# Performance work log

Hardware: AMD Instinct MI355X
Metric: run time of the kernel (lower is better)

## Reference

```python
import jax, jax.numpy as jnp
import numpy as np

F, H, D, A, B = 500, 2000, 64, 64, 4096


def setup_inputs() -> dict:
    key = jax.random.key(0)
    ks = jax.random.split(key, 6)
    values = jax.random.normal(ks[0], (B, F), dtype=jnp.float32)
    feat_emb = jax.random.normal(ks[1], (F, D), dtype=jnp.float32) * 0.02
    hid_emb = jax.random.normal(ks[2], (H, D), dtype=jnp.float32) * 0.02
    Ww = jax.random.normal(ks[3], (2 * D, A), dtype=jnp.float32) * (1.0 / np.sqrt(2 * D))
    bw = jnp.zeros((A,), dtype=jnp.float32)
    Wu = jax.random.normal(ks[4], (A, 1), dtype=jnp.float32) * (1.0 / np.sqrt(A))
    mask = jax.random.bernoulli(ks[5], 0.1, (F, F + H, 1))
    return {"values": values, "feat_emb": feat_emb, "hid_emb": hid_emb,
            "Ww": Ww, "bw": bw, "Wu": Wu, "mask": mask}


def reference(values, feat_emb, hid_emb, Ww, bw, Wu, mask):
    d = feat_emb.shape[1]
    # full embedding matrix: concat(feature, hidden) -> [F+H, d]
    full = jnp.concatenate([feat_emb, hid_emb], axis=0)
    # Dense(tanh) on concat([feat_emb tiled, full tiled], axis=2) == split-weight form:
    # avoids materializing the [F, F+H, 2d] concat tensor (same math).
    W1, W2 = Ww[:d], Ww[d:]
    pre_f = feat_emb @ W1          # [F, A]
    pre_w = full @ W2              # [F+H, A]
    h = jnp.tanh(pre_f[:, None, :] + pre_w[None, :, :] + bw)  # [F, F+H, A]
    score = h @ Wu                 # [F, F+H, 1]
    # masked exp-normalize (not a stable softmax: original uses raw exp)
    score = jnp.where(mask, jnp.exp(score), 0.0)
    ssum = jnp.sum(score, axis=1, keepdims=True)        # [F, 1, 1]
    ssum = jnp.where(ssum == 0, 1.0, ssum)
    attn = score / ssum                                  # [F, F+H, 1]
    context = jnp.sum(attn * full[None, :, :], axis=1)   # [F, d]
    return values @ context                              # [B, d]
```

## Files before the change

kernel.cpp:

```cpp
#include <hip/hip_runtime.h>
#include <cstdint>
#include <cstddef>

#define F_N 500
#define H_N 2000
#define JN  2500
#define D_N 64
#define A_N 64
#define B_N 4096

__global__ __launch_bounds__(256) void k_pre(
    const float* __restrict__ feat, const float* __restrict__ hid,
    const float* __restrict__ Ww,   const float* __restrict__ bw,
    float* __restrict__ pre_f, float* __restrict__ pre_w)
{
    const int lane = threadIdx.x & 63;
    const int wave = threadIdx.x >> 6;
    const int row  = blockIdx.x * 4 + wave;
    if (row >= F_N + JN) return;

    const float* emb;
    const float* W;
    float*       outp;
    float        acc = 0.0f;

    if (row < F_N) {
        emb  = feat + (size_t)row * D_N;
        W    = Ww;
        outp = pre_f + (size_t)row * A_N;
        acc  = bw[lane];
    } else {
        const int j = row - F_N;
        emb  = (j < F_N) ? (feat + (size_t)j * D_N)
                         : (hid + (size_t)(j - F_N) * D_N);
        W    = Ww + D_N * A_N;
        outp = pre_w + (size_t)j * A_N;
    }

    const float e = emb[lane];
    #pragma unroll 16
    for (int d = 0; d < D_N; ++d) {
        const float w = W[d * A_N + lane];
        const float b = __shfl(e, d, 64);
        acc = fmaf(b, w, acc);
    }
    outp[lane] = acc;
}

__global__ __launch_bounds__(256) void k_attn(
    const float* __restrict__ feat, const float* __restrict__ hid,
    const float* __restrict__ pre_f, const float* __restrict__ pre_w,
    const float* __restrict__ Wu,   const void* __restrict__ mask,
    float* __restrict__ ctx)
{
    const int lane = threadIdx.x & 63;
    const int wave = threadIdx.x >> 6;
    const int i    = blockIdx.x;

    const uint32_t* mw = (const uint32_t*)mask;
    const uint32_t probe = mw[lane] | mw[64 + lane] | mw[128 + lane] | mw[192 + lane];
    const bool byteMode = (__ballot(probe > 1u) != 0ull);

    const float pf = pre_f[(size_t)i * A_N + lane];
    const float wu = Wu[lane];

    const uint8_t*  mb = (const uint8_t*)mask + (size_t)i * JN;
    const uint32_t* mi = (const uint32_t*)mask + (size_t)i * JN;

    float cacc = 0.0f;
    float sacc = 0.0f;

    for (int c = wave; c < 40; c += 4) {
        const int j0 = c * 64;
        const int j  = j0 + lane;
        uint32_t m = 0;
        if (j < JN) m = byteMode ? (uint32_t)mb[j] : mi[j];
        unsigned long long act = __ballot(m != 0);

        while (act) {
            const int b0 = __builtin_ctzll(act); act &= act - 1;
            const bool has1 = (act != 0ull);
            const int b1 = has1 ? __builtin_ctzll(act) : b0;
            if (has1) act &= act - 1;
            const int jj0 = j0 + b0;
            const int jj1 = j0 + b1;

            const float x0 = pf + pre_w[(size_t)jj0 * A_N + lane];
            const float x1 = pf + pre_w[(size_t)jj1 * A_N + lane];
            const float t0 = 1.0f - 2.0f / (__expf(2.0f * x0) + 1.0f);
            const float t1 = 1.0f - 2.0f / (__expf(2.0f * x1) + 1.0f);
            float p0 = t0 * wu;
            float p1 = t1 * wu;
            #pragma unroll
            for (int off = 1; off < 64; off <<= 1) {
                p0 += __shfl_xor(p0, off, 64);
                p1 += __shfl_xor(p1, off, 64);
            }
            const float e0 = __expf(p0);
            const float e1 = has1 ? __expf(p1) : 0.0f;
            sacc += e0 + e1;

            const float f0 = (jj0 < F_N) ? feat[(size_t)jj0 * D_N + lane]
                                         : hid[(size_t)(jj0 - F_N) * D_N + lane];
            const float f1 = (jj1 < F_N) ? feat[(size_t)jj1 * D_N + lane]
                                         : hid[(size_t)(jj1 - F_N) * D_N + lane];
            cacc = fmaf(e0, f0, cacc);
            cacc = fmaf(e1, f1, cacc);
        }
    }

    __shared__ float s_ctx[4][64];
    __shared__ float s_sum[4];
    s_ctx[wave][lane] = cacc;
    if (lane == 0) s_sum[wave] = sacc;
    __syncthreads();
    if (wave == 0) {
        const float c4 = s_ctx[0][lane] + s_ctx[1][lane] + s_ctx[2][lane] + s_ctx[3][lane];
        float s = s_sum[0] + s_sum[1] + s_sum[2] + s_sum[3];
        if (s == 0.0f) s = 1.0f;
        ctx[(size_t)i * D_N + lane] = c4 / s;
    }
}

__global__ __launch_bounds__(256) void k_out(
    const float* __restrict__ values, const float* __restrict__ ctx,
    float* __restrict__ out)
{
    const int lane = threadIdx.x & 63;
    const int wave = threadIdx.x >> 6;
    const int row0 = blockIdx.x * 8 + wave * 2;

    __shared__ float lds[100 * 64];
    float acc0 = 0.0f, acc1 = 0.0f;

    for (int chunk = 0; chunk < 5; ++chunk) {
        const int k0 = chunk * 100;
        __syncthreads();
        for (int t = threadIdx.x; t < 100 * 64; t += 256)
            lds[t] = ctx[(size_t)k0 * 64 + t];
        __syncthreads();

        const float* v0p = values + (size_t)row0 * 500 + k0;
        const float* v1p = v0p + 500;
        #pragma unroll 5
        for (int kc = 0; kc < 100; kc += 4) {
            const float4 a = *(const float4*)(v0p + kc);
            const float4 b = *(const float4*)(v1p + kc);
            const float l0 = lds[(kc + 0) * 64 + lane];
            const float l1 = lds[(kc + 1) * 64 + lane];
            const float l2 = lds[(kc + 2) * 64 + lane];
            const float l3 = lds[(kc + 3) * 64 + lane];
            acc0 = fmaf(a.x, l0, acc0); acc0 = fmaf(a.y, l1, acc0);
            acc0 = fmaf(a.z, l2, acc0); acc0 = fmaf(a.w, l3, acc0);
            acc1 = fmaf(b.x, l0, acc1); acc1 = fmaf(b.y, l1, acc1);
            acc1 = fmaf(b.z, l2, acc1); acc1 = fmaf(b.w, l3, acc1);
        }
    }
    out[(size_t)row0 * 64 + lane]       = acc0;
    out[(size_t)(row0 + 1) * 64 + lane] = acc1;
}

extern "C" void kernel_launch(void* const* d_in, const int* in_sizes, int n_in,
                              void* d_out, int out_size, void* d_ws, size_t ws_size,
                              hipStream_t stream)
{
    const float* values = (const float*)d_in[0];
    const float* feat   = (const float*)d_in[1];
    const float* hid    = (const float*)d_in[2];
    const float* Ww     = (const float*)d_in[3];
    const float* bw     = (const float*)d_in[4];
    const float* Wu     = (const float*)d_in[5];
    const void*  mask   = d_in[6];
    float* out = (float*)d_out;

    float* wsf   = (float*)d_ws;
    float* pre_f = wsf;
    float* pre_w = wsf + 32000;
    float* ctx   = wsf + 192000;

    k_pre <<<750, 256, 0, stream>>>(feat, hid, Ww, bw, pre_f, pre_w);
    k_attn<<<500, 256, 0, stream>>>(feat, hid, pre_f, pre_w, Wu, mask, ctx);
    k_out <<<512, 256, 0, stream>>>(values, ctx, out);
}
```

Measured before the change: 132.5 us.

## Transpose pre_w and compute attention scores one-per-thread over compacted mask list

k_pre now has each wave compute four rows and writes pre_w transposed through an LDS tile. k_attn first compacts the active mask indices into a shared list using ballot and atomics. Each thread then computes a full 64-wide tanh score for one active index, reading pre_w with coalesced transposed loads, instead of doing a wave-wide shuffle reduction per index. This removes the per-index butterfly reductions and the serial per-wave loop, at the cost of extra LDS use, more synchronization, and a nondeterministic list order that changes the float summation order.

```diff
diff --git a/kernel.cpp b/kernel.cpp
--- a/kernel.cpp
+++ b/kernel.cpp
@@ -9,116 +9,152 @@
 #define A_N 64
 #define B_N 4096
 
-__global__ __launch_bounds__(256) void k_pre(
+__global__ __launch_bounds__(1024) void k_pre(
     const float* __restrict__ feat, const float* __restrict__ hid,
     const float* __restrict__ Ww,   const float* __restrict__ bw,
-    float* __restrict__ pre_f, float* __restrict__ pre_w)
+    float* __restrict__ pre_f, float* __restrict__ pre_wT)
 {
     const int lane = threadIdx.x & 63;
     const int wave = threadIdx.x >> 6;
-    const int row  = blockIdx.x * 4 + wave;
-    if (row >= F_N + JN) return;
-
-    const float* emb;
-    const float* W;
-    float*       outp;
-    float        acc = 0.0f;
-
-    if (row < F_N) {
-        emb  = feat + (size_t)row * D_N;
-        W    = Ww;
-        outp = pre_f + (size_t)row * A_N;
-        acc  = bw[lane];
-    } else {
-        const int j = row - F_N;
-        emb  = (j < F_N) ? (feat + (size_t)j * D_N)
-                         : (hid + (size_t)(j - F_N) * D_N);
-        W    = Ww + D_N * A_N;
-        outp = pre_w + (size_t)j * A_N;
-    }
-
-    const float e = emb[lane];
-    #pragma unroll 16
+
+    __shared__ float tile[64 * 65];
+
+    const bool isPreF = (blockIdx.x < 8);
+    const int  rbase  = isPreF ? blockIdx.x * 64 : (blockIdx.x - 8) * 64;
+    const int  r0     = rbase + wave * 4;
+    const int  rowLim = isPreF ? F_N : JN;
+
+    const float* W = isPreF ? Ww : (Ww + D_N * A_N);
+
+    float acc0, acc1, acc2, acc3;
+    if (isPreF) { const float b = bw[lane]; acc0 = acc1 = acc2 = acc3 = b; }
+    else        { acc0 = acc1 = acc2 = acc3 = 0.0f; }
+
+    float e0 = 0.f, e1 = 0.f, e2 = 0.f, e3 = 0.f;
+    {
+        const int r[4] = { r0, r0 + 1, r0 + 2, r0 + 3 };
+        float* ep[4] = { &e0, &e1, &e2, &e3 };
+        #pragma unroll
+        for (int q = 0; q < 4; ++q) {
+            const int rr = r[q];
+            if (rr < rowLim) {
+                const float* emb;
+                if (isPreF)          emb = feat + (size_t)rr * D_N;
+                else if (rr < F_N)   emb = feat + (size_t)rr * D_N;
+                else                 emb = hid + (size_t)(rr - F_N) * D_N;
+                *ep[q] = emb[lane];
+            }
+        }
+    }
+
+    #pragma unroll
     for (int d = 0; d < D_N; ++d) {
         const float w = W[d * A_N + lane];
-        const float b = __shfl(e, d, 64);
-        acc = fmaf(b, w, acc);
-    }
-    outp[lane] = acc;
+        acc0 = fmaf(__shfl(e0, d, 64), w, acc0);
+        acc1 = fmaf(__shfl(e1, d, 64), w, acc1);
+        acc2 = fmaf(__shfl(e2, d, 64), w, acc2);
+        acc3 = fmaf(__shfl(e3, d, 64), w, acc3);
+    }
+
+    if (isPreF) {
+        if (r0 + 0 < F_N) pre_f[(size_t)(r0 + 0) * A_N + lane] = acc0;
+        if (r0 + 1 < F_N) pre_f[(size_t)(r0 + 1) * A_N + lane] = acc1;
+        if (r0 + 2 < F_N) pre_f[(size_t)(r0 + 2) * A_N + lane] = acc2;
+        if (r0 + 3 < F_N) pre_f[(size_t)(r0 + 3) * A_N + lane] = acc3;
+    } else {
+        const int l0 = wave * 4;
+        tile[(l0 + 0) * 65 + lane] = acc0;
+        tile[(l0 + 1) * 65 + lane] = acc1;
+        tile[(l0 + 2) * 65 + lane] = acc2;
+        tile[(l0 + 3) * 65 + lane] = acc3;
+        __syncthreads();
+        #pragma unroll
+        for (int k = 0; k < 4; ++k) {
+            const int idx = threadIdx.x + k * 1024;
+            const int a   = idx >> 6;
+            const int jj  = idx & 63;
+            const int j   = rbase + jj;
+            if (j < JN)
+                pre_wT[(size_t)a * JN + j] = tile[jj * 65 + a];
+        }
+    }
 }
 
 __global__ __launch_bounds__(256) void k_attn(
     const float* __restrict__ feat, const float* __restrict__ hid,
-    const float* __restrict__ pre_f, const float* __restrict__ pre_w,
+    const float* __restrict__ pre_f, const float* __restrict__ pre_wT,
     const float* __restrict__ Wu,   const void* __restrict__ mask,
     float* __restrict__ ctx)
 {
-    const int lane = threadIdx.x & 63;
-    const int wave = threadIdx.x >> 6;
+    const int tid  = threadIdx.x;
+    const int lane = tid & 63;
+    const int wave = tid >> 6;
     const int i    = blockIdx.x;
+
+    __shared__ int   list[JN];
+    __shared__ float earr[JN];
+    __shared__ float s_ctx[4][64];
+    __shared__ int   nact;
+
+    if (tid == 0) nact = 0;
+    __syncthreads();
 
     const uint32_t* mw = (const uint32_t*)mask;
     const uint32_t probe = mw[lane] | mw[64 + lane] | mw[128 + lane] | mw[192 + lane];
     const bool byteMode = (__ballot(probe > 1u) != 0ull);
 
-    const float pf = pre_f[(size_t)i * A_N + lane];
-    const float wu = Wu[lane];
-
     const uint8_t*  mb = (const uint8_t*)mask + (size_t)i * JN;
     const uint32_t* mi = (const uint32_t*)mask + (size_t)i * JN;
 
+    for (int t = tid; t < 2560; t += 256) {
+        uint32_t m = 0;
+        if (t < JN) m = byteMode ? (uint32_t)mb[t] : mi[t];
+        const unsigned long long act = __ballot(m != 0);
+        const int cnt = __popcll(act);
+        int base = 0;
+        if (lane == 0 && cnt) base = atomicAdd(&nact, cnt);
+        base = __shfl(base, 0, 64);
+        if (m) {
+            const int rank = __popcll(act & ((1ull << lane) - 1ull));
+            list[base + rank] = t;
+        }
+    }
+    __syncthreads();
+    const int n = nact;
+
+    const float* pf = pre_f + (size_t)i * A_N;
+    for (int idx = tid; idx < n; idx += 256) {
+        const int j = list[idx];
+        float s = 0.0f;
+        #pragma unroll 8
+        for (int a = 0; a < A_N; ++a) {
+            const float x = pf[a] + pre_wT[(size_t)a * JN + j];
+            const float t = 1.0f - 2.0f / (__expf(2.0f * x) + 1.0f);
+            s = fmaf(Wu[a], t, s);
+        }
+        earr[idx] = __expf(s);
+    }
+    __syncthreads();
+
     float cacc = 0.0f;
-    float sacc = 0.0f;
-
-    for (int c = wave; c < 40; c += 4) {
-        const int j0 = c * 64;
-        const int j  = j0 + lane;
-        uint32_t m = 0;
-        if (j < JN) m = byteMode ? (uint32_t)mb[j] : mi[j];
-        unsigned long long act = __ballot(m != 0);
-
-        while (act) {
-            const int b0 = __builtin_ctzll(act); act &= act - 1;
-            const bool has1 = (act != 0ull);
-            const int b1 = has1 ? __builtin_ctzll(act) : b0;
-            if (has1) act &= act - 1;
-            const int jj0 = j0 + b0;
-            const int jj1 = j0 + b1;
-
-            const float x0 = pf + pre_w[(size_t)jj0 * A_N + lane];
-            const float x1 = pf + pre_w[(size_t)jj1 * A_N + lane];
-            const float t0 = 1.0f - 2.0f / (__expf(2.0f * x0) + 1.0f);
-            const float t1 = 1.0f - 2.0f / (__expf(2.0f * x1) + 1.0f);
-            float p0 = t0 * wu;
-            float p1 = t1 * wu;
-            #pragma unroll
-            for (int off = 1; off < 64; off <<= 1) {
-                p0 += __shfl_xor(p0, off, 64);
-                p1 += __shfl_xor(p1, off, 64);
-            }
-            const float e0 = __expf(p0);
-            const float e1 = has1 ? __expf(p1) : 0.0f;
-            sacc += e0 + e1;
-
-            const float f0 = (jj0 < F_N) ? feat[(size_t)jj0 * D_N + lane]
-                                         : hid[(size_t)(jj0 - F_N) * D_N + lane];
-            const float f1 = (jj1 < F_N) ? feat[(size_t)jj1 * D_N + lane]
-                                         : hid[(size_t)(jj1 - F_N) * D_N + lane];
-            cacc = fmaf(e0, f0, cacc);
-            cacc = fmaf(e1, f1, cacc);
-        }
-    }
-
-    __shared__ float s_ctx[4][64];
-    __shared__ float s_sum[4];
+    for (int idx = wave; idx < n; idx += 4) {
+        const float e = earr[idx];
+        const int   j = list[idx];
+        const float* row = (j < F_N) ? (feat + (size_t)j * D_N)
+                                     : (hid + (size_t)(j - F_N) * D_N);
+        cacc = fmaf(e, row[lane], cacc);
+    }
     s_ctx[wave][lane] = cacc;
-    if (lane == 0) s_sum[wave] = sacc;
-    __syncthreads();
+    __syncthreads();
+
     if (wave == 0) {
         const float c4 = s_ctx[0][lane] + s_ctx[1][lane] + s_ctx[2][lane] + s_ctx[3][lane];
-        float s = s_sum[0] + s_sum[1] + s_sum[2] + s_sum[3];
-        if (s == 0.0f) s = 1.0f;
-        ctx[(size_t)i * D_N + lane] = c4 / s;
+        float ss = 0.0f;
+        for (int k = lane; k < n; k += 64) ss += earr[k];
+        #pragma unroll
+        for (int off = 1; off < 64; off <<= 1) ss += __shfl_xor(ss, off, 64);
+        if (ss == 0.0f) ss = 1.0f;
+        ctx[(size_t)i * D_N + lane] = c4 / ss;
     }
 }
 
@@ -173,12 +209,12 @@
     const void*  mask   = d_in[6];
     float* out = (float*)d_out;
 
-    float* wsf   = (float*)d_ws;
-    float* pre_f = wsf;
-    float* pre_w = wsf + 32000;
-    float* ctx   = wsf + 192000;
-
-    k_pre <<<750, 256, 0, stream>>>(feat, hid, Ww, bw, pre_f, pre_w);
-    k_attn<<<500, 256, 0, stream>>>(feat, hid, pre_f, pre_w, Wu, mask, ctx);
+    float* wsf    = (float*)d_ws;
+    float* pre_f  = wsf;
+    float* pre_wT = wsf + 32000;
+    float* ctx    = wsf + 192000;
+
+    k_pre <<<48, 1024, 0, stream>>>(feat, hid, Ww, bw, pre_f, pre_wT);
+    k_attn<<<500, 256, 0, stream>>>(feat, hid, pre_f, pre_wT, Wu, mask, ctx);
     k_out <<<512, 256, 0, stream>>>(values, ctx, out);
 }
```

After: 144.6 us. 9.1% more time.

## Compact active mask entries and compute attention scores per-thread instead of per-wave

Applied to the files above, without the earlier changes.

The attention kernel now builds a compacted list of active (masked-in) columns in shared memory using ballot and atomic offsets. Each thread then computes one full score, a 64-wide tanh dot product over a float4-loaded pre_w row, instead of a wave cooperatively computing one score with a 6-step shuffle reduction. This removes the cross-lane reductions and serialized ctz loops, at the cost of per-thread strided row reads and about 20KB of extra LDS per block. The exp-sum is recomputed from the stored scores, and the small projection kernel loop is fully unrolled.

```diff
diff --git a/kernel.cpp b/kernel.cpp
--- a/kernel.cpp
+++ b/kernel.cpp
@@ -38,11 +38,10 @@
     }
 
     const float e = emb[lane];
-    #pragma unroll 16
+    #pragma unroll
     for (int d = 0; d < D_N; ++d) {
         const float w = W[d * A_N + lane];
-        const float b = __shfl(e, d, 64);
-        acc = fmaf(b, w, acc);
+        acc = fmaf(__shfl(e, d, 64), w, acc);
     }
     outp[lane] = acc;
 }
@@ -53,72 +52,87 @@
     const float* __restrict__ Wu,   const void* __restrict__ mask,
     float* __restrict__ ctx)
 {
-    const int lane = threadIdx.x & 63;
-    const int wave = threadIdx.x >> 6;
+    const int tid  = threadIdx.x;
+    const int lane = tid & 63;
+    const int wave = tid >> 6;
     const int i    = blockIdx.x;
+
+    __shared__ int   list[JN];
+    __shared__ float earr[JN];
+    __shared__ float s_ctx[4][64];
+    __shared__ int   nact;
+
+    if (tid == 0) nact = 0;
+    __syncthreads();
 
     const uint32_t* mw = (const uint32_t*)mask;
     const uint32_t probe = mw[lane] | mw[64 + lane] | mw[128 + lane] | mw[192 + lane];
     const bool byteMode = (__ballot(probe > 1u) != 0ull);
 
-    const float pf = pre_f[(size_t)i * A_N + lane];
-    const float wu = Wu[lane];
-
     const uint8_t*  mb = (const uint8_t*)mask + (size_t)i * JN;
     const uint32_t* mi = (const uint32_t*)mask + (size_t)i * JN;
 
-    float cacc = 0.0f;
-    float sacc = 0.0f;
+    for (int t = tid; t < 2560; t += 256) {
+        uint32_t m = 0;
+        if (t < JN) m = byteMode ? (uint32_t)mb[t] : mi[t];
+        const unsigned long long act = __ballot(m != 0);
+        const int cnt = __popcll(act);
+        int base = 0;
+        if (lane == 0 && cnt) base = atomicAdd(&nact, cnt);
+        base = __shfl(base, 0, 64);
+        if (m) {
+            const int rank = __popcll(act & ((1ull << lane) - 1ull));
+            list[base + rank] = t;
+        }
+    }
+    __syncthreads();
+    const int n = nact;
 
-    for (int c = wave; c < 40; c += 4) {
-        const int j0 = c * 64;
-        const int j  = j0 + lane;
-        uint32_t m = 0;
-        if (j < JN) m = byteMode ? (uint32_t)mb[j] : mi[j];
-        unsigned long long act = __ballot(m != 0);
-
-        while (act) {
-            const int b0 = __builtin_ctzll(act); act &= act - 1;
-            const bool has1 = (act != 0ull);
-            const int b1 = has1 ? __builtin_ctzll(act) : b0;
-            if (has1) act &= act - 1;
-            const int jj0 = j0 + b0;
-            const int jj1 = j0 + b1;
-
-            const float x0 = pf + pre_w[(size_t)jj0 * A_N + lane];
-            const float x1 = pf + pre_w[(size_t)jj1 * A_N + lane];
+    const float* pf = pre_f + (size_t)i * A_N;
+    for (int idx = tid; idx < n; idx += 256) {
+        const int j = list[idx];
+        const float4* pwj = (const float4*)(pre_w + (size_t)j * A_N);
+        float s = 0.0f;
+        #pragma unroll
+        for (int q = 0; q < 16; ++q) {
+            const float4 v = pwj[q];
+            const int a = q * 4;
+            const float x0 = pf[a + 0] + v.x;
+            const float x1 = pf[a + 1] + v.y;
+            const float x2 = pf[a + 2] + v.z;
+            const float x3 = pf[a + 3] + v.w;
             const float t0 = 1.0f - 2.0f / (__expf(2.0f * x0) + 1.0f);
             const float t1 = 1.0f - 2.0f / (__expf(2.0f * x1) + 1.0f);
-            float p0 = t0 * wu;
-            float p1 = t1 * wu;
-            #pragma unroll
-            for (int off = 1; off < 64; off <<= 1) {
-                p0 += __shfl_xor(p0, off, 64);
-                p1 += __shfl_xor(p1, off, 64);
-            }
-            const float e0 = __expf(p0);
-            const float e1 = has1 ? __expf(p1) : 0.0f;
-            sacc += e0 + e1;
+            const float t2 = 1.0f - 2.0f / (__expf(2.0f * x2) + 1.0f);
+            const float t3 = 1.0f - 2.0f / (__expf(2.0f * x3) + 1.0f);
+            s = fmaf(Wu[a + 0], t0, s);
+            s = fmaf(Wu[a + 1], t1, s);
+            s = fmaf(Wu[a + 2], t2, s);
+            s = fmaf(Wu[a + 3], t3, s);
+        }
+        earr[idx] = __expf(s);
+    }
+    __syncthreads();
 
-            const float f0 = (jj0 < F_N) ? feat[(size_t)jj0 * D_N + lane]
-                                         : hid[(size_t)(jj0 - F_N) * D_N + lane];
-            const float f1 = (jj1 < F_N) ? feat[(size_t)jj1 * D_N + lane]
-                                         : hid[(size_t)(jj1 - F_N) * D_N + lane];
-            cacc = fmaf(e0, f0, cacc);
-            cacc = fmaf(e1, f1, cacc);
-        }
+    float cacc = 0.0f;
+    for (int idx = wave; idx < n; idx += 4) {
+        const float e = earr[idx];
+        const int   j = list[idx];
+        const float* row = (j < F_N) ? (feat + (size_t)j * D_N)
+                                     : (hid + (size_t)(j - F_N) * D_N);
+        cacc = fmaf(e, row[lane], cacc);
     }
+    s_ctx[wave][lane] = cacc;
+    __syncthreads();
 
-    __shared__ float s_ctx[4][64];
-    __shared__ float s_sum[4];
-    s_ctx[wave][lane] = cacc;
-    if (lane == 0) s_sum[wave] = sacc;
-    __syncthreads();
     if (wave == 0) {
         const float c4 = s_ctx[0][lane] + s_ctx[1][lane] + s_ctx[2][lane] + s_ctx[3][lane];
-        float s = s_sum[0] + s_sum[1] + s_sum[2] + s_sum[3];
-        if (s == 0.0f) s = 1.0f;
-        ctx[(size_t)i * D_N + lane] = c4 / s;
+        float ss = 0.0f;
+        for (int k = lane; k < n; k += 64) ss += earr[k];
+        #pragma unroll
+        for (int off = 1; off < 64; off <<= 1) ss += __shfl_xor(ss, off, 64);
+        if (ss == 0.0f) ss = 1.0f;
+        ctx[(size_t)i * D_N + lane] = c4 / ss;
     }
 }
 
```

New measurement: 132.2 us. Within noise of the previous version (-0.2%).
